# Kernel optimization log

Measured on AMD Instinct MI355X. Metric: run time of the kernel, lower is better.

Reference implementation:

```python
import jax, jax.numpy as jnp
import numpy as np

N_NODES = 100000
N_EDGES = 1600000
IN_FEATS = 256
N_HEADS = 4
OUT_FEATS = 32
NEG_SLOPE = 0.2


def setup_inputs() -> dict:
    key = jax.random.key(0)
    k0, k1, k2, k3, k4, k5 = jax.random.split(key, 6)
    feat = jax.random.normal(k0, (N_NODES, IN_FEATS), dtype=jnp.float32)
    src = jax.random.randint(k1, (N_EDGES,), 0, N_NODES, dtype=jnp.int32)
    dst = jax.random.randint(k2, (N_EDGES,), 0, N_NODES, dtype=jnp.int32)
    # fc.weight: [num_heads*out_feats, in_feats] (torch Linear layout)
    W = jax.random.normal(k3, (N_HEADS * OUT_FEATS, IN_FEATS), dtype=jnp.float32) * 0.05
    attn_l = jax.random.normal(k4, (1, N_HEADS, OUT_FEATS), dtype=jnp.float32) * 0.1
    attn_r = jax.random.normal(k5, (1, N_HEADS, OUT_FEATS), dtype=jnp.float32) * 0.1
    return {"feat": feat, "src": src, "dst": dst, "W": W, "attn_l": attn_l, "attn_r": attn_r}


def reference(feat, src, dst, W, attn_l, attn_r):
    N = feat.shape[0]
    H, D = attn_l.shape[1], attn_l.shape[2]
    # fc projection -> [N, H, D]
    feat_src = (feat @ W.T).reshape(N, H, D)
    el = jnp.sum(feat_src * attn_l, axis=-1)  # [N, H]
    er = jnp.sum(feat_src * attn_r, axis=-1)  # [N, H]
    # per-edge scores: u_add_v then LeakyReLU  -> [E, H]
    e = jax.nn.leaky_relu(el[src] + er[dst], negative_slope=NEG_SLOPE)
    # edge_softmax: segmented softmax over edges grouped by destination node
    emax = jax.ops.segment_max(e, dst, num_segments=N)  # [N, H]
    emax = jnp.where(jnp.isfinite(emax), emax, jnp.zeros_like(emax))
    ee = jnp.exp(e - emax[dst])  # [E, H]
    denom = jax.ops.segment_sum(ee, dst, num_segments=N)  # [N, H]
    a = ee / denom[dst]  # [E, H]
    # u_mul_e + sum aggregation -> [N, H, D]
    m = feat_src[src] * a[:, :, None]  # [E, H, D]
    rst = jax.ops.segment_sum(m, dst, num_segments=N)
    return rst
```

## Files before the change

kernel.cpp:

```cpp
#include <hip/hip_runtime.h>
#include <hip/hip_bf16.h>
#include <math.h>

#define NN 100000
#define NE 1600000
#define INF_ 256
#define NH 4
#define DH 32
#define NHD 128
#define NEG_SLOPE 0.2f

#define NB3 1563
#define STRIDE 1280
#define EPB 4096
#define NBLK_BIN 391
#define GEMM_BLKS 782
#define SMEM_BYTES 32768

typedef __attribute__((ext_vector_type(8))) short bf16x8;
typedef __attribute__((ext_vector_type(4))) float f32x4;

__device__ __forceinline__ unsigned short f2bf(float f) {
    __hip_bfloat16 b = __float2bfloat16(f);
    return *reinterpret_cast<unsigned short*>(&b);
}

__global__ __launch_bounds__(256) void k_prep0(const float* __restrict__ W,
                                               unsigned short* __restrict__ Wimg,
                                               int* __restrict__ gcurP) {
    int t = threadIdx.x;
    int b = blockIdx.x;
    if (b == 16) {
        for (int i = t; i < NB3; i += 256) gcurP[i * 16] = 0;
        return;
    }
    int i = b * 256 + t;
    int kt = i >> 9;
    int r = (i >> 2) & 127;
    int g = i & 3;
    int slot = g ^ (r & 7);
    const float* s = &W[(size_t)r * INF_ + kt * 32 + g * 8];
    unsigned short tmp[8];
#pragma unroll
    for (int j = 0; j < 8; j++) tmp[j] = f2bf(s[j]);
    *(bf16x8*)&Wimg[(size_t)kt * 8192 + r * 64 + slot * 8] = *(const bf16x8*)tmp;
}

__global__ __launch_bounds__(256) void k_gemmbin(const float* __restrict__ feat,
                                                 const unsigned short* __restrict__ Wimg,
                                                 const int* __restrict__ src,
                                                 const int* __restrict__ dst,
                                                 const float* __restrict__ al,
                                                 const float* __restrict__ ar,
                                                 unsigned short* __restrict__ fsb,
                                                 float* __restrict__ el,
                                                 float* __restrict__ er,
                                                 int* __restrict__ gcurP,
                                                 unsigned* __restrict__ packed) {
    __shared__ __align__(16) char smem[SMEM_BYTES];
    const int t = threadIdx.x;

    if (blockIdx.x >= GEMM_BLKS) {
        int hb = blockIdx.x - GEMM_BLKS;
        int* ldst = (int*)smem;
        int* lc = (int*)(smem + EPB * 4);
        int* wb = (int*)(smem + EPB * 4 + NB3 * 4);
        for (int i = t; i < NB3; i += 256) lc[i] = 0;
        __syncthreads();
        int base = hb * EPB;
#pragma unroll
        for (int j = 0; j < 16; j++) {
            int e = base + j * 256 + t;
            int d = (e < NE) ? dst[e] : -1;
            ldst[j * 256 + t] = d;
            if (d >= 0) atomicAdd(&lc[d >> 6], 1);
        }
        __syncthreads();
        for (int i = t; i < NB3; i += 256) {
            int c = lc[i];
            wb[i] = c ? i * STRIDE + atomicAdd(&gcurP[i * 16], c) : 0;
            lc[i] = 0;
        }
        __syncthreads();
#pragma unroll
        for (int j = 0; j < 16; j++) {
            int e = base + j * 256 + t;
            if (e < NE) {
                int d = ldst[j * 256 + t];
                int bk = d >> 6;
                int pos = wb[bk] + atomicAdd(&lc[bk], 1);
                if (pos < (bk + 1) * STRIDE)
                    packed[pos] = ((unsigned)src[e] << 6) | (unsigned)(d & 63);
            }
        }
        return;
    }

    short* sA = (short*)smem;
    short* sB = (short*)(smem + 16384);
    const int brow = blockIdx.x * 128;
    const int wid = t >> 6, lane = t & 63;
    const int wr = wid >> 1, wc = wid & 1;
    const int lg = lane >> 4;
    const int lr = lane & 15;

    f32x4 acc[4][4];
#pragma unroll
    for (int m = 0; m < 4; m++)
#pragma unroll
        for (int n = 0; n < 4; n++) acc[m][n] = (f32x4){0.f, 0.f, 0.f, 0.f};

    const int srow = t >> 1;
    const int cb = (t & 1) * 16;
    const int g0 = cb >> 3;
    const int p0 = (g0 ^ (srow & 7));
    const int p1 = ((g0 + 1) ^ (srow & 7));
    const int grow = brow + srow;
    const bool arow_ok = (grow < NN);
    const char* bimg = (const char*)Wimg;

    float fv[16];
    uint4 wv0, wv1, wv2, wv3;
    if (arow_ok) {
        const float4* pa = (const float4*)&feat[(size_t)grow * INF_ + cb];
        *(float4*)&fv[0] = pa[0];
        *(float4*)&fv[4] = pa[1];
        *(float4*)&fv[8] = pa[2];
        *(float4*)&fv[12] = pa[3];
    } else {
#pragma unroll
        for (int j = 0; j < 16; j++) fv[j] = 0.f;
    }
    wv0 = *(const uint4*)(bimg + t * 16);
    wv1 = *(const uint4*)(bimg + 4096 + t * 16);
    wv2 = *(const uint4*)(bimg + 8192 + t * 16);
    wv3 = *(const uint4*)(bimg + 12288 + t * 16);

    for (int kt = 0; kt < 8; kt++) {
        {
            short sv[16];
#pragma unroll
            for (int j = 0; j < 16; j++) sv[j] = (short)f2bf(fv[j]);
            *(bf16x8*)&sA[srow * 64 + p0 * 8] = *(const bf16x8*)&sv[0];
            *(bf16x8*)&sA[srow * 64 + p1 * 8] = *(const bf16x8*)&sv[8];
            char* bd = (char*)sB;
            *(uint4*)(bd + t * 16) = wv0;
            *(uint4*)(bd + 4096 + t * 16) = wv1;
            *(uint4*)(bd + 8192 + t * 16) = wv2;
            *(uint4*)(bd + 12288 + t * 16) = wv3;
        }
        __syncthreads();
        if (kt < 7) {
            int k0 = (kt + 1) * 32;
            if (arow_ok) {
                const float4* pa = (const float4*)&feat[(size_t)grow * INF_ + k0 + cb];
                *(float4*)&fv[0] = pa[0];
                *(float4*)&fv[4] = pa[1];
                *(float4*)&fv[8] = pa[2];
                *(float4*)&fv[12] = pa[3];
            }
            const char* bsrc = bimg + (size_t)(kt + 1) * 16384;
            wv0 = *(const uint4*)(bsrc + t * 16);
            wv1 = *(const uint4*)(bsrc + 4096 + t * 16);
            wv2 = *(const uint4*)(bsrc + 8192 + t * 16);
            wv3 = *(const uint4*)(bsrc + 12288 + t * 16);
        }
        bf16x8 aF[4], bF[4];
#pragma unroll
        for (int m = 0; m < 4; m++) {
            int r = wr * 64 + m * 16 + lr;
            aF[m] = *(const bf16x8*)&sA[r * 64 + ((lg ^ (r & 7)) * 8)];
        }
#pragma unroll
        for (int n = 0; n < 4; n++) {
            int r = wc * 64 + n * 16 + lr;
            bF[n] = *(const bf16x8*)&sB[r * 64 + ((lg ^ (r & 7)) * 8)];
        }
#pragma unroll
        for (int m = 0; m < 4; m++)
#pragma unroll
            for (int n = 0; n < 4; n++)
                acc[m][n] = __builtin_amdgcn_mfma_f32_16x16x32_bf16(aF[m], bF[n], acc[m][n], 0, 0, 0);
        __syncthreads();
    }
#pragma unroll
    for (int m = 0; m < 4; m++) {
#pragma unroll
        for (int n = 0; n < 4; n++) {
#pragma unroll
            for (int r = 0; r < 4; r++) {
                int gr = brow + wr * 64 + m * 16 + lg * 4 + r;
                if (gr < NN)
                    fsb[(size_t)gr * NHD + wc * 64 + n * 16 + lr] = f2bf(acc[m][n][r]);
            }
        }
    }
    const int hA = wc * 2, hB = wc * 2 + 1;
    const float alA0 = al[hA * 32 + lr], alA1 = al[hA * 32 + 16 + lr];
    const float alB0 = al[hB * 32 + lr], alB1 = al[hB * 32 + 16 + lr];
    const float arA0 = ar[hA * 32 + lr], arA1 = ar[hA * 32 + 16 + lr];
    const float arB0 = ar[hB * 32 + lr], arB1 = ar[hB * 32 + 16 + lr];
#pragma unroll
    for (int m = 0; m < 4; m++) {
#pragma unroll
        for (int r = 0; r < 4; r++) {
            float eA = acc[m][0][r] * alA0 + acc[m][1][r] * alA1;
            float eB = acc[m][2][r] * alB0 + acc[m][3][r] * alB1;
            float fA = acc[m][0][r] * arA0 + acc[m][1][r] * arA1;
            float fB = acc[m][2][r] * arB0 + acc[m][3][r] * arB1;
#pragma unroll
            for (int off = 1; off < 16; off <<= 1) {
                eA += __shfl_xor(eA, off);
                eB += __shfl_xor(eB, off);
                fA += __shfl_xor(fA, off);
                fB += __shfl_xor(fB, off);
            }
            if (lr == 0) {
                int gr = brow + wr * 64 + m * 16 + lg * 4 + r;
                if (gr < NN) {
                    el[gr * 4 + hA] = eA;
                    el[gr * 4 + hB] = eB;
                    er[gr * 4 + hA] = fA;
                    er[gr * 4 + hB] = fB;
                }
            }
        }
    }
}

__global__ __launch_bounds__(256) void k_sortagg(const int* __restrict__ gcurP,
                                                 const unsigned* __restrict__ packed,
                                                 const float* __restrict__ el,
                                                 const float* __restrict__ er,
                                                 const uint4* __restrict__ fsb128,
                                                 float* __restrict__ out) {
    __shared__ int lh[64];
    __shared__ int off[65];
    __shared__ int cur[64];
    __shared__ int esrc_l[STRIDE];
    int b = blockIdx.x, t = threadIdx.x;
    int beg = b * STRIDE;
    int cnt = gcurP[b * 16];
    if (cnt > STRIDE) cnt = STRIDE;

    if (t < 64) lh[t] = 0;
    __syncthreads();
    for (int k = t; k < cnt; k += 256)
        atomicAdd(&lh[packed[beg + k] & 63u], 1);
    __syncthreads();
    if (t < 64) {
        int v = lh[t];
        int x = v;
#pragma unroll
        for (int o = 1; o < 64; o <<= 1) {
            int y = __shfl_up(x, o);
            if (t >= o) x += y;
        }
        off[t] = x - v;
        cur[t] = x - v;
        if (t == 63) off[64] = x;
    }
    __syncthreads();
    for (int k = t; k < cnt; k += 256) {
        unsigned p = packed[beg + k];
        int pos = atomicAdd(&cur[p & 63u], 1);
        esrc_l[pos] = (int)(p >> 6);
    }
    __syncthreads();

    int lane = t & 63;
    int wv = t >> 6;
    int q = lane >> 4;
    int sl = lane & 15;
    int h = sl >> 2;

#define STEP(eV, vV)                                           \
    {                                                          \
        float sc_ = (eV) + rr;                                 \
        sc_ = sc_ > 0.f ? sc_ : NEG_SLOPE * sc_;               \
        float ee = __expf(sc_);                                \
        den += ee;                                             \
        a0 += ee * __uint_as_float((vV).x << 16);              \
        a1 += ee * __uint_as_float((vV).x & 0xFFFF0000u);      \
        a2 += ee * __uint_as_float((vV).y << 16);              \
        a3 += ee * __uint_as_float((vV).y & 0xFFFF0000u);      \
        a4 += ee * __uint_as_float((vV).z << 16);              \
        a5 += ee * __uint_as_float((vV).z & 0xFFFF0000u);      \
        a6 += ee * __uint_as_float((vV).w << 16);              \
        a7 += ee * __uint_as_float((vV).w & 0xFFFF0000u);      \
    }

    for (int ln = wv * 16; ln < wv * 16 + 16; ln++) {
        int node = (b << 6) + ln;
        if (node >= NN) break;
        int bg = off[ln];
        int en = off[ln + 1];
        float rr = er[node * 4 + h];
        float den = 0.f;
        float a0 = 0.f, a1 = 0.f, a2 = 0.f, a3 = 0.f;
        float a4 = 0.f, a5 = 0.f, a6 = 0.f, a7 = 0.f;
        int k = bg + q;
        for (; k + 4 < en; k += 8) {
            int s0 = esrc_l[k];
            int s1 = esrc_l[k + 4];
            uint4 v0 = fsb128[(size_t)s0 * 16 + sl];
            uint4 v1 = fsb128[(size_t)s1 * 16 + sl];
            float e0 = el[s0 * 4 + h];
            float e1 = el[s1 * 4 + h];
            STEP(e0, v0)
            STEP(e1, v1)
        }
        for (; k < en; k += 4) {
            int s = esrc_l[k];
            uint4 vv = fsb128[(size_t)s * 16 + sl];
            float eV = el[s * 4 + h];
            STEP(eV, vv)
        }
#pragma unroll
        for (int o = 16; o <= 32; o <<= 1) {
            a0 += __shfl_xor(a0, o);
            a1 += __shfl_xor(a1, o);
            a2 += __shfl_xor(a2, o);
            a3 += __shfl_xor(a3, o);
            a4 += __shfl_xor(a4, o);
            a5 += __shfl_xor(a5, o);
            a6 += __shfl_xor(a6, o);
            a7 += __shfl_xor(a7, o);
            den += __shfl_xor(den, o);
        }
        if (q == 0) {
            float inv = den > 0.f ? 1.0f / den : 0.f;
            float4 o0, o1;
            o0.x = a0 * inv; o0.y = a1 * inv; o0.z = a2 * inv; o0.w = a3 * inv;
            o1.x = a4 * inv; o1.y = a5 * inv; o1.z = a6 * inv; o1.w = a7 * inv;
            float* p = &out[(size_t)node * NHD + sl * 8];
            *(float4*)p = o0;
            *(float4*)(p + 4) = o1;
        }
    }
#undef STEP
}

extern "C" void kernel_launch(void* const* d_in, const int* in_sizes, int n_in,
                              void* d_out, int out_size, void* d_ws, size_t ws_size,
                              hipStream_t stream) {
    const float* feat = (const float*)d_in[0];
    const int* src = (const int*)d_in[1];
    const int* dst = (const int*)d_in[2];
    const float* W = (const float*)d_in[3];
    const float* al = (const float*)d_in[4];
    const float* ar = (const float*)d_in[5];
    float* out = (float*)d_out;

    char* ws = (char*)d_ws;
    unsigned short* fsb = (unsigned short*)ws;   ws += (size_t)NN * NHD * 2;
    unsigned* packed = (unsigned*)ws;            ws += (size_t)NB3 * STRIDE * 4;
    float* el = (float*)ws;                      ws += (size_t)NN * NH * 4;
    float* er = (float*)ws;                      ws += (size_t)NN * NH * 4;
    int* gcurP = (int*)ws;                       ws += (size_t)NB3 * 16 * 4;
    unsigned short* Wimg = (unsigned short*)ws;  ws += (size_t)8 * 8192 * 2;

    k_prep0<<<17, 256, 0, stream>>>(W, Wimg, gcurP);
    k_gemmbin<<<GEMM_BLKS + NBLK_BIN, 256, 0, stream>>>(feat, Wimg, src, dst,
                                                        al, ar, fsb, el, er,
                                                        gcurP, packed);
    k_sortagg<<<NB3, 256, 0, stream>>>(gcurP, packed, el, er,
                                       (const uint4*)fsb, out);
}
```

Baseline: 151.9 us.

## Coarsen destination buckets to 256 nodes and split aggregation into quarter-blocks

Binning now groups edges into 391 coarse buckets of 256 destination nodes instead of 1563 buckets of 64, which means fewer global atomics and better write locality per bin block. Each bin block handles 8192 edges and rereads dst from global memory rather than staging it in shared memory. The aggregation kernel launches four blocks per coarse bucket. Each block scans the whole bucket and keeps only the edges whose destinations fall in its 64-node quarter, so every block reads four times as much packed data. It also adds FMAX truncation guards that could drop edges if a quarter is unusually dense.

```diff
diff --git a/kernel.cpp b/kernel.cpp
--- a/kernel.cpp
+++ b/kernel.cpp
@@ -10,11 +10,12 @@
 #define NHD 128
 #define NEG_SLOPE 0.2f
 
-#define NB3 1563
-#define STRIDE 1280
-#define EPB 4096
-#define NBLK_BIN 391
+#define NBC 391
+#define STRIDEC 4608
+#define EPBC 8192
+#define NBLK_BIN 196
 #define GEMM_BLKS 782
+#define FMAX 1408
 #define SMEM_BYTES 32768
 
 typedef __attribute__((ext_vector_type(8))) short bf16x8;
@@ -31,7 +32,7 @@
     int t = threadIdx.x;
     int b = blockIdx.x;
     if (b == 16) {
-        for (int i = t; i < NB3; i += 256) gcurP[i * 16] = 0;
+        for (int i = t; i < NBC; i += 256) gcurP[i * 16] = 0;
         return;
     }
     int i = b * 256 + t;
@@ -62,35 +63,32 @@
 
     if (blockIdx.x >= GEMM_BLKS) {
         int hb = blockIdx.x - GEMM_BLKS;
-        int* ldst = (int*)smem;
-        int* lc = (int*)(smem + EPB * 4);
-        int* wb = (int*)(smem + EPB * 4 + NB3 * 4);
-        for (int i = t; i < NB3; i += 256) lc[i] = 0;
-        __syncthreads();
-        int base = hb * EPB;
-#pragma unroll
-        for (int j = 0; j < 16; j++) {
+        int* lc = (int*)smem;
+        int* wb = ((int*)smem) + NBC;
+        for (int i = t; i < NBC; i += 256) lc[i] = 0;
+        __syncthreads();
+        int base = hb * EPBC;
+#pragma unroll 4
+        for (int j = 0; j < 32; j++) {
             int e = base + j * 256 + t;
-            int d = (e < NE) ? dst[e] : -1;
-            ldst[j * 256 + t] = d;
-            if (d >= 0) atomicAdd(&lc[d >> 6], 1);
-        }
-        __syncthreads();
-        for (int i = t; i < NB3; i += 256) {
+            if (e < NE) atomicAdd(&lc[dst[e] >> 8], 1);
+        }
+        __syncthreads();
+        for (int i = t; i < NBC; i += 256) {
             int c = lc[i];
-            wb[i] = c ? i * STRIDE + atomicAdd(&gcurP[i * 16], c) : 0;
+            wb[i] = c ? i * STRIDEC + atomicAdd(&gcurP[i * 16], c) : 0;
             lc[i] = 0;
         }
         __syncthreads();
-#pragma unroll
-        for (int j = 0; j < 16; j++) {
+#pragma unroll 4
+        for (int j = 0; j < 32; j++) {
             int e = base + j * 256 + t;
             if (e < NE) {
-                int d = ldst[j * 256 + t];
-                int bk = d >> 6;
+                int d = dst[e];
+                int bk = d >> 8;
                 int pos = wb[bk] + atomicAdd(&lc[bk], 1);
-                if (pos < (bk + 1) * STRIDE)
-                    packed[pos] = ((unsigned)src[e] << 6) | (unsigned)(d & 63);
+                if (pos < (bk + 1) * STRIDEC)
+                    packed[pos] = ((unsigned)src[e] << 8) | (unsigned)(d & 255);
             }
         }
         return;
@@ -237,16 +235,20 @@
     __shared__ int lh[64];
     __shared__ int off[65];
     __shared__ int cur[64];
-    __shared__ int esrc_l[STRIDE];
-    int b = blockIdx.x, t = threadIdx.x;
-    int beg = b * STRIDE;
+    __shared__ int esrc_l[FMAX];
+    int bq = blockIdx.x;
+    int b = bq >> 2, quarter = bq & 3;
+    int t = threadIdx.x;
+    int beg = b * STRIDEC;
     int cnt = gcurP[b * 16];
-    if (cnt > STRIDE) cnt = STRIDE;
+    if (cnt > STRIDEC) cnt = STRIDEC;
 
     if (t < 64) lh[t] = 0;
     __syncthreads();
-    for (int k = t; k < cnt; k += 256)
-        atomicAdd(&lh[packed[beg + k] & 63u], 1);
+    for (int k = t; k < cnt; k += 256) {
+        unsigned p = packed[beg + k];
+        if (((p >> 6) & 3u) == (unsigned)quarter) atomicAdd(&lh[p & 63u], 1);
+    }
     __syncthreads();
     if (t < 64) {
         int v = lh[t];
@@ -263,8 +265,10 @@
     __syncthreads();
     for (int k = t; k < cnt; k += 256) {
         unsigned p = packed[beg + k];
-        int pos = atomicAdd(&cur[p & 63u], 1);
-        esrc_l[pos] = (int)(p >> 6);
+        if (((p >> 6) & 3u) == (unsigned)quarter) {
+            int pos = atomicAdd(&cur[p & 63u], 1);
+            if (pos < FMAX) esrc_l[pos] = (int)(p >> 8);
+        }
     }
     __syncthreads();
 
@@ -291,10 +295,11 @@
     }
 
     for (int ln = wv * 16; ln < wv * 16 + 16; ln++) {
-        int node = (b << 6) + ln;
+        int node = (b << 8) + (quarter << 6) + ln;
         if (node >= NN) break;
         int bg = off[ln];
         int en = off[ln + 1];
+        if (en > FMAX) en = FMAX;
         float rr = er[node * 4 + h];
         float den = 0.f;
         float a0 = 0.f, a1 = 0.f, a2 = 0.f, a3 = 0.f;
@@ -354,16 +359,16 @@
 
     char* ws = (char*)d_ws;
     unsigned short* fsb = (unsigned short*)ws;   ws += (size_t)NN * NHD * 2;
-    unsigned* packed = (unsigned*)ws;            ws += (size_t)NB3 * STRIDE * 4;
+    unsigned* packed = (unsigned*)ws;            ws += (size_t)NBC * STRIDEC * 4;
     float* el = (float*)ws;                      ws += (size_t)NN * NH * 4;
     float* er = (float*)ws;                      ws += (size_t)NN * NH * 4;
-    int* gcurP = (int*)ws;                       ws += (size_t)NB3 * 16 * 4;
+    int* gcurP = (int*)ws;                       ws += (size_t)NBC * 16 * 4;
     unsigned short* Wimg = (unsigned short*)ws;  ws += (size_t)8 * 8192 * 2;
 
     k_prep0<<<17, 256, 0, stream>>>(W, Wimg, gcurP);
     k_gemmbin<<<GEMM_BLKS + NBLK_BIN, 256, 0, stream>>>(feat, Wimg, src, dst,
                                                         al, ar, fsb, el, er,
                                                         gcurP, packed);
-    k_sortagg<<<NB3, 256, 0, stream>>>(gcurP, packed, el, er,
-                                       (const uint4*)fsb, out);
-}
+    k_sortagg<<<NBC * 4, 256, 0, stream>>>(gcurP, packed, el, er,
+                                           (const uint4*)fsb, out);
+}
```

Measured after the change: 151.5 us. No clear change (-0.2%).
